# Performance work log

Hardware: AMD Instinct MI355X
Metric: run time of the kernel (lower is better)

The kernel has to match this reference:

```python
import jax, jax.numpy as jnp
import numpy as np

EPS = 1e-5
L = 8      # n_layers
H = 1024   # n_hidden
F_IN = 26  # input features
B = 65536  # batch


def layer_norm(x, gamma, beta):
    m = jnp.mean(x, axis=-1, keepdims=True)
    v = jnp.mean((x - m) ** 2, axis=-1, keepdims=True)
    return (x - m) * jax.lax.rsqrt(v + EPS) * gamma + beta


def setup_inputs() -> dict:
    key = jax.random.key(0)
    ks = jax.random.split(key, 12)
    s_in = 1.0 / np.sqrt(F_IN)
    s_h = 1.0 / np.sqrt(H)
    return {
        "x": jax.random.normal(ks[0], (B, F_IN), jnp.float32),
        "st_gamma": jnp.ones((F_IN,), jnp.float32),
        "st_beta": jnp.zeros((F_IN,), jnp.float32),
        "st_w": jax.random.uniform(ks[1], (H, F_IN), jnp.float32, -s_in, s_in),
        "st_b": jax.random.uniform(ks[2], (H,), jnp.float32, -s_in, s_in),
        "blk_gamma": jnp.ones((L, H), jnp.float32),
        "blk_beta": jnp.zeros((L, H), jnp.float32),
        "blk_w": jax.random.uniform(ks[3], (L, H, H), jnp.float32, -s_h, s_h),
        "blk_b": jax.random.uniform(ks[4], (L, H), jnp.float32, -s_h, s_h),
        "last_gamma": jnp.ones((H,), jnp.float32),
        "last_beta": jnp.zeros((H,), jnp.float32),
        "last_w": jax.random.uniform(ks[5], (1, H), jnp.float32, -s_h, s_h),
        "last_b": jax.random.uniform(ks[6], (1,), jnp.float32, -s_h, s_h),
    }


def reference(x, st_gamma, st_beta, st_w, st_b,
              blk_gamma, blk_beta, blk_w, blk_b,
              last_gamma, last_beta, last_w, last_b):
    # Stem: LN(26) -> Linear(26->H) -> ReLU (dropout = identity in eval)
    h = jax.nn.relu(layer_norm(x, st_gamma, st_beta) @ st_w.T + st_b)

    # n_layers blocks: LN -> Linear(H->H) -> ReLU, scanned over stacked params
    def body(h, params):
        g, b, w, bb = params
        h = jax.nn.relu(layer_norm(h, g, b) @ w.T + bb)
        return h, None

    h, _ = jax.lax.scan(body, h, (blk_gamma, blk_beta, blk_w, blk_b))

    # Head: LN -> Linear(H->1) -> sigmoid
    h = layer_norm(h, last_gamma, last_beta)
    out = jax.nn.sigmoid(h @ last_w.T + last_b)  # [B, 1]
    return out
```

## Files before the change

kernel.cpp:

```cpp
#include <hip/hip_runtime.h>
#include <hip/hip_bf16.h>
#include <stdint.h>


typedef __attribute__((ext_vector_type(8))) _Float16 f16x8;
typedef __attribute__((ext_vector_type(4))) float f32x4;

#define EPSLN 1e-5f
#define HDIM 1024

__device__ __forceinline__ void gload16(const void* g, void* l) {
  __builtin_amdgcn_global_load_lds(
      (const __attribute__((address_space(1))) unsigned int*)g,
      (__attribute__((address_space(3))) unsigned int*)l, 16, 0, 0);
}

__global__ __launch_bounds__(256) void zero_f32(float* __restrict__ p, int n) {
  int i = blockIdx.x * 256 + threadIdx.x;
  if (i < n) p[i] = 0.f;
}

__global__ __launch_bounds__(256) void fold_blk(
    const float* __restrict__ bg, const float* __restrict__ bb,
    const float* __restrict__ bw, const float* __restrict__ bbias,
    float* __restrict__ bfold, float* __restrict__ Sfold) {
  int lo = blockIdx.x;
  int layer = lo >> 10;
  const float* wrow = bw + (size_t)lo * HDIM;
  const float* g = bg + (size_t)layer * HDIM;
  const float* be = bb + (size_t)layer * HDIM;
  int t = threadIdx.x;
  float s = 0.f, acb = 0.f;
  for (int i = t; i < HDIM; i += 256) {
    float wv = wrow[i];
    _Float16 wp = (_Float16)(wv * g[i]);
    s += (float)wp;
    acb += be[i] * wv;
  }
#pragma unroll
  for (int off = 1; off < 64; off <<= 1) { s += __shfl_xor(s, off); acb += __shfl_xor(acb, off); }
  __shared__ float rs[4], rb[4];
  int l = t & 63, w = t >> 6;
  if (l == 0) { rs[w] = s; rb[w] = acb; }
  __syncthreads();
  if (t == 0) {
    Sfold[lo] = rs[0] + rs[1] + rs[2] + rs[3];
    bfold[lo] = bbias[lo] + rb[0] + rb[1] + rb[2] + rb[3];
  }
}

__global__ __launch_bounds__(256) void fold_pack(
    const float* __restrict__ bg, const float* __restrict__ bw,
    _Float16* __restrict__ Wfrag) {
  size_t tid = (size_t)blockIdx.x * 256 + threadIdx.x;
  int lay = (int)(tid >> 17);
  int oct = (int)(tid & 131071);
  int frag = oct >> 6, lane = oct & 63;
  int n16 = frag >> 5, kc = frag & 31;
  int o = n16 * 16 + (lane & 15);
  int ibase = kc * 32 + ((lane >> 4) << 3);
  const float* wrow = bw + ((size_t)lay << 20) + (size_t)o * HDIM + ibase;
  const float* g = bg + (size_t)lay * HDIM + ibase;
  f16x8 v;
#pragma unroll
  for (int j = 0; j < 8; ++j) v[j] = (_Float16)(wrow[j] * g[j]);
  *(f16x8*)(Wfrag + tid * 8) = v;
}

__global__ __launch_bounds__(256) void fold_head(
    const float* __restrict__ lg, const float* __restrict__ lb,
    const float* __restrict__ lw, const float* __restrict__ lbias,
    float* __restrict__ headW, float* __restrict__ headAux) {
  int t = threadIdx.x;
  float s = 0.f, acb = 0.f;
  for (int i = t; i < HDIM; i += 256) {
    float wp = lw[i] * lg[i];
    headW[i] = wp;
    s += wp;
    acb += lb[i] * lw[i];
  }
#pragma unroll
  for (int off = 1; off < 64; off <<= 1) { s += __shfl_xor(s, off); acb += __shfl_xor(acb, off); }
  __shared__ float rs[4], rb[4];
  int l = t & 63, w = t >> 6;
  if (l == 0) { rs[w] = s; rb[w] = acb; }
  __syncthreads();
  if (t == 0) {
    headAux[0] = rs[0] + rs[1] + rs[2] + rs[3];
    headAux[1] = lbias[0] + rb[0] + rb[1] + rb[2] + rb[3];
  }
}

__global__ __launch_bounds__(256) void fold_stem(const float* __restrict__ stw,
                                                 _Float16* __restrict__ Wst) {
  int idx = blockIdx.x * 256 + threadIdx.x;
  int o = idx >> 6, j = idx & 63;
  int i = (((j >> 3) ^ (o & 7)) << 3) + (j & 7);
  Wst[idx] = (i < 26) ? (_Float16)stw[o * 26 + i] : (_Float16)0.f;
}

__global__ __launch_bounds__(256) void stem_gemm(
    const float* __restrict__ x, const float* __restrict__ stg, const float* __restrict__ stb,
    const _Float16* __restrict__ Wst, const float* __restrict__ stbias,
    _Float16* __restrict__ hout, float* __restrict__ stats_out, int rowBase) {
  __shared__ float xin[128 * 26];
  __shared__ _Float16 As[128 * 64];
  __shared__ _Float16 Bs[128 * 64];
  const int t = threadIdx.x;
  const int l = t & 63;
  const int w = t >> 6;
  const int wm = w >> 1, wn = w & 1;
  const int brow = blockIdx.x * 128;
  const int bcol = blockIdx.y * 128;

  const _Float16* gb = Wst + (size_t)(bcol + (t >> 3)) * 64 + (t & 7) * 8;
  char* lB = (char*)Bs + (size_t)w * 1024;
#pragma unroll
  for (int q = 0; q < 4; ++q) gload16(gb + (size_t)q * 32 * 64, lB + q * 4096);

  const float* src = x + ((size_t)rowBase + brow) * 26;
  for (int i = t; i < 128 * 26; i += 256) xin[i] = src[i];
  __syncthreads();

  if (t < 128) {
    float m = 0.f;
#pragma unroll
    for (int i = 0; i < 26; ++i) m += xin[t * 26 + i];
    m *= (1.f / 26.f);
    float v = 0.f;
#pragma unroll
    for (int i = 0; i < 26; ++i) { float d = xin[t * 26 + i] - m; v += d * d; }
    float rstd = rsqrtf(v * (1.f / 26.f) + EPSLN);
    _Float16 tmp[32];
#pragma unroll
    for (int i = 0; i < 26; ++i)
      tmp[i] = (_Float16)((xin[t * 26 + i] - m) * rstd * stg[i] + stb[i]);
#pragma unroll
    for (int i = 26; i < 32; ++i) tmp[i] = (_Float16)0.f;
    char* arow = (char*)As + t * 128;
#pragma unroll
    for (int c = 0; c < 4; ++c) {
      f16x8 vv;
#pragma unroll
      for (int j = 0; j < 8; ++j) vv[j] = tmp[c * 8 + j];
      *(f16x8*)(arow + ((c ^ (t & 7)) << 4)) = vv;
    }
    f16x8 vz = (f16x8)(_Float16)0.f;
#pragma unroll
    for (int c = 4; c < 8; ++c) *(f16x8*)(arow + ((c ^ (t & 7)) << 4)) = vz;
  }
  __syncthreads();

  f32x4 acc[4][4];
#pragma unroll
  for (int i = 0; i < 4; ++i)
#pragma unroll
    for (int j = 0; j < 4; ++j) acc[i][j] = (f32x4){0.f, 0.f, 0.f, 0.f};

#pragma unroll
  for (int ks = 0; ks < 2; ++ks) {
    const int cx = ((ks * 4 + (l >> 4)) ^ (l & 7)) << 4;
    f16x8 af[4], bfr[4];
#pragma unroll
    for (int m = 0; m < 4; ++m)
      af[m] = *(const f16x8*)((const char*)As + (wm * 64 + m * 16 + (l & 15)) * 128 + cx);
#pragma unroll
    for (int n = 0; n < 4; ++n)
      bfr[n] = *(const f16x8*)((const char*)Bs + (wn * 64 + n * 16 + (l & 15)) * 128 + cx);
#pragma unroll
    for (int m = 0; m < 4; ++m)
#pragma unroll
      for (int n = 0; n < 4; ++n)
        acc[m][n] = __builtin_amdgcn_mfma_f32_16x16x32_f16(af[m], bfr[n], acc[m][n], 0, 0, 0);
  }

  __syncthreads();
  float* sred = (float*)xin;
  if (t < 256) sred[t] = 0.f;
  __syncthreads();

  float Bf[4];
#pragma unroll
  for (int n = 0; n < 4; ++n) Bf[n] = stbias[bcol + wn * 64 + n * 16 + (l & 15)];
#pragma unroll
  for (int m = 0; m < 4; ++m) {
#pragma unroll
    for (int rg = 0; rg < 4; ++rg) {
      int rloc = wm * 64 + m * 16 + (l >> 4) * 4 + rg;
      int lrow = brow + rloc;
      float ps = 0.f, psq = 0.f;
#pragma unroll
      for (int n = 0; n < 4; ++n) {
        int col = bcol + wn * 64 + n * 16 + (l & 15);
        float vv = fmaxf(acc[m][n][rg] + Bf[n], 0.f);
        hout[(size_t)lrow * HDIM + col] = (_Float16)vv;
        ps += vv; psq += vv * vv;
      }
#pragma unroll
      for (int off = 1; off < 16; off <<= 1) {
        ps += __shfl_xor(ps, off);
        psq += __shfl_xor(psq, off);
      }
      if ((l & 15) == 0) {
        atomicAdd(&sred[rloc * 2 + 0], ps);
        atomicAdd(&sred[rloc * 2 + 1], psq);
      }
    }
  }
  __syncthreads();
  if (t < 256) atomicAdd(&stats_out[(size_t)(brow + (t >> 1)) * 2 + (t & 1)], sred[t]);
}

__global__ __launch_bounds__(256, 2) void layer_gemm(
    const _Float16* __restrict__ hin, const float* __restrict__ stats_in,
    const _Float16* __restrict__ Wfrag, const float* __restrict__ bfold,
    const float* __restrict__ Sfold, _Float16* __restrict__ hout,
    float* __restrict__ stats_out) {
  __shared__ __align__(128) char smem[2 * 8192];
  const int t = threadIdx.x;
  const int l = t & 63;
  const int w = t >> 6;
  const int wn = w;
  int bid = blockIdx.x;
  {
    int nb = gridDim.x;
    if ((nb & 7) == 0) { int cpx = nb >> 3; bid = (bid & 7) * cpx + (bid >> 3); }
  }
  const int brow = (bid >> 2) * 128;
  const int bcol = (bid & 3) * 256;

  f32x4 acc[8][4];
#pragma unroll
  for (int i = 0; i < 8; ++i)
#pragma unroll
    for (int j = 0; j < 4; ++j) acc[i][j] = (f32x4){0.f, 0.f, 0.f, 0.f};

  const int cswz = (t & 3) ^ ((t >> 3) & 3);
  const _Float16* gA = hin + (size_t)(brow + (t >> 2)) * HDIM + cswz * 8;
  const int dstw = w << 10;

  auto stageA = [&](int kt) {
    char* dA = smem + (kt & 1) * 8192 + dstw;
    const _Float16* sA = gA + kt * 32;
    gload16(sA, dA);
    gload16(sA + (size_t)64 * HDIM, dA + 4096);
  };

  const _Float16* gBf = Wfrag + ((size_t)((bcol >> 4) + wn * 4) * 2048 + l) * 8;

  const int rl = l & 15;
  const int cx = (((l >> 4) ^ ((rl >> 1) & 3)) << 4);
  const int arow0 = rl * 64 + cx;

  f16x8 af[8], bf0[4], bf1[4];

#define LOADB(kt, dst)                                                         \
  do {                                                                         \
    _Pragma("unroll") for (int n = 0; n < 4; ++n)                              \
        dst[n] = *(const f16x8*)(gBf + (size_t)n * 16384 + (kt) * 512);        \
  } while (0)
#define DS_AF(kt)                                                              \
  do {                                                                         \
    const char* bc = smem + ((kt) & 1) * 8192;                                 \
    _Pragma("unroll") for (int m = 0; m < 8; ++m)                              \
        af[m] = *(const f16x8*)(bc + arow0 + m * 1024);                        \
  } while (0)
#define MFMA32(src)                                                            \
  do {                                                                         \
    __builtin_amdgcn_s_setprio(1);                                             \
    _Pragma("unroll") for (int m = 0; m < 8; ++m)                              \
        _Pragma("unroll") for (int n = 0; n < 4; ++n)                          \
            acc[m][n] = __builtin_amdgcn_mfma_f32_16x16x32_f16(af[m], src[n],  \
                                                               acc[m][n], 0, 0, 0); \
    __builtin_amdgcn_s_setprio(0);                                             \
  } while (0)
#define WAIT_PRE(N)                                                            \
  do {                                                                         \
    asm volatile("s_waitcnt vmcnt(" #N ") lgkmcnt(0)" ::: "memory");           \
    __builtin_amdgcn_sched_barrier(0);                                         \
  } while (0)
#define BOUNDARY()                                                             \
  do {                                                                         \
    __builtin_amdgcn_sched_barrier(0);                                         \
    asm volatile("s_waitcnt vmcnt(4)" ::: "memory");                           \
    __builtin_amdgcn_s_barrier();                                              \
    __builtin_amdgcn_sched_barrier(0);                                         \
  } while (0)

  stageA(0);
  LOADB(0, bf0);
  asm volatile("s_waitcnt vmcnt(4)" ::: "memory");
  __builtin_amdgcn_s_barrier();
  __builtin_amdgcn_sched_barrier(0);

#pragma unroll 1
  for (int kt2 = 0; kt2 < 15; ++kt2) {
    const int kt = kt2 * 2;
    stageA(kt + 1);
    LOADB(kt + 1, bf1);
    DS_AF(kt);
    WAIT_PRE(6);
    MFMA32(bf0);
    BOUNDARY();
    stageA(kt + 2);
    LOADB(kt + 2, bf0);
    DS_AF(kt + 1);
    WAIT_PRE(6);
    MFMA32(bf1);
    BOUNDARY();
  }
  stageA(31);
  LOADB(31, bf1);
  DS_AF(30);
  WAIT_PRE(6);
  MFMA32(bf0);
  BOUNDARY();
  DS_AF(31);
  WAIT_PRE(0);
  MFMA32(bf1);
  __syncthreads();

#undef LOADB
#undef DS_AF
#undef MFMA32
#undef WAIT_PRE
#undef BOUNDARY

  float* sred = (float*)smem;
  sred[t] = 0.f;
  __syncthreads();

  float Sf[4], Bf2[4];
#pragma unroll
  for (int n = 0; n < 4; ++n) {
    int col = bcol + wn * 64 + n * 16 + rl;
    Sf[n] = Sfold[col];
    Bf2[n] = bfold[col];
  }
#pragma unroll
  for (int m = 0; m < 8; ++m) {
#pragma unroll
    for (int rg = 0; rg < 4; ++rg) {
      int rloc = m * 16 + (l >> 4) * 4 + rg;
      int grow = brow + rloc;
      float sum = stats_in[(size_t)grow * 2 + 0];
      float sumsq = stats_in[(size_t)grow * 2 + 1];
      float mean = sum * (1.f / 1024.f);
      float rstd = rsqrtf(sumsq * (1.f / 1024.f) - mean * mean + EPSLN);
      float ps = 0.f, psq = 0.f;
#pragma unroll
      for (int n = 0; n < 4; ++n) {
        int col = bcol + wn * 64 + n * 16 + rl;
        float vv = rstd * (acc[m][n][rg] - mean * Sf[n]) + Bf2[n];
        vv = fmaxf(vv, 0.f);
        hout[(size_t)grow * HDIM + col] = (_Float16)vv;
        ps += vv; psq += vv * vv;
      }
#pragma unroll
      for (int off2 = 1; off2 < 16; off2 <<= 1) {
        ps += __shfl_xor(ps, off2);
        psq += __shfl_xor(psq, off2);
      }
      if (rl == 0) {
        atomicAdd(&sred[rloc * 2 + 0], ps);
        atomicAdd(&sred[rloc * 2 + 1], psq);
      }
    }
  }
  __syncthreads();
  atomicAdd(&stats_out[(size_t)(brow + (t >> 1)) * 2 + (t & 1)], sred[t]);
}

__global__ __launch_bounds__(512) void head_kernel(
    const _Float16* __restrict__ h8, const float* __restrict__ stats8,
    const float* __restrict__ headW, const float* __restrict__ headAux,
    float* __restrict__ out, int rowBase) {
  int t = threadIdx.x, l = t & 63, w = t >> 6;
  int lrow = blockIdx.x * 8 + w;
  const f16x8* hp = (const f16x8*)(h8 + (size_t)lrow * HDIM) + l * 2;
  f16x8 v0 = hp[0], v1 = hp[1];
  float acc = 0.f;
#pragma unroll
  for (int j = 0; j < 8; ++j) acc += (float)v0[j] * headW[l * 16 + j];
#pragma unroll
  for (int j = 0; j < 8; ++j) acc += (float)v1[j] * headW[l * 16 + 8 + j];
#pragma unroll
  for (int off = 1; off < 64; off <<= 1) acc += __shfl_xor(acc, off);
  if (l == 0) {
    float sum = stats8[lrow * 2 + 0], sumsq = stats8[lrow * 2 + 1];
    float mean = sum * (1.f / 1024.f);
    float rstd = rsqrtf(sumsq * (1.f / 1024.f) - mean * mean + EPSLN);
    float z = rstd * (acc - mean * headAux[0]) + headAux[1];
    out[rowBase + lrow] = 1.f / (1.f + expf(-z));
  }
}

extern "C" void kernel_launch(void* const* d_in, const int* in_sizes, int n_in,
                              void* d_out, int out_size, void* d_ws, size_t ws_size,
                              hipStream_t stream) {
  const float* x      = (const float*)d_in[0];
  const float* stg    = (const float*)d_in[1];
  const float* stb    = (const float*)d_in[2];
  const float* stw    = (const float*)d_in[3];
  const float* stbias = (const float*)d_in[4];
  const float* bg     = (const float*)d_in[5];
  const float* bb     = (const float*)d_in[6];
  const float* bw     = (const float*)d_in[7];
  const float* bbias  = (const float*)d_in[8];
  const float* lg     = (const float*)d_in[9];
  const float* lb     = (const float*)d_in[10];
  const float* lw     = (const float*)d_in[11];
  const float* lbias  = (const float*)d_in[12];
  float* out = (float*)d_out;
  const int B = 65536;
  const int L = 8;

  char* ws = (char*)d_ws;
  size_t off = 0;
  auto carve = [&](size_t bytes) -> char* {
    char* p = ws + off;
    off = (off + bytes + 255) & ~(size_t)255;
    return p;
  };
  _Float16* Wfrag = (_Float16*)carve((size_t)L * HDIM * HDIM * 2);
  float* bfold   = (float*)carve((size_t)L * HDIM * 4);
  float* Sfold   = (float*)carve((size_t)L * HDIM * 4);
  float* headW   = (float*)carve((size_t)HDIM * 4);
  float* headAux = (float*)carve(256);
  _Float16* Wst  = (_Float16*)carve((size_t)HDIM * 64 * 2);
  size_t fixed = off;

  int R = B;
  while (R > 256) {
    size_t need = fixed + 2 * ((size_t)R * HDIM * 2 + 256) + ((size_t)9 * R * 2 * 4 + 256);
    if (need <= ws_size) break;
    R >>= 1;
  }
  _Float16* hA = (_Float16*)carve((size_t)R * HDIM * 2);
  _Float16* hB = (_Float16*)carve((size_t)R * HDIM * 2);
  float* stats = (float*)carve((size_t)9 * R * 2 * 4);

  fold_blk<<<L * HDIM, 256, 0, stream>>>(bg, bb, bw, bbias, bfold, Sfold);
  fold_pack<<<(L * 131072) / 256, 256, 0, stream>>>(bg, bw, Wfrag);
  fold_head<<<1, 256, 0, stream>>>(lg, lb, lw, lbias, headW, headAux);
  fold_stem<<<HDIM * 64 / 256, 256, 0, stream>>>(stw, Wst);

  const int nstats = 9 * R * 2;
  for (int c = 0; c < B / R; ++c) {
    int rowBase = c * R;
    zero_f32<<<(nstats + 255) / 256, 256, 0, stream>>>(stats, nstats);
    {
      dim3 grid(R / 128, 8);
      stem_gemm<<<grid, 256, 0, stream>>>(x, stg, stb, Wst, stbias, hA, stats, rowBase);
    }
    _Float16* cur = hA;
    _Float16* nxt = hB;
    for (int lyr = 0; lyr < L; ++lyr) {
      int nb = (R / 128) * 4;
      layer_gemm<<<nb, 256, 0, stream>>>(
          cur, stats + (size_t)lyr * R * 2, Wfrag + (size_t)lyr * HDIM * HDIM,
          bfold + lyr * HDIM, Sfold + lyr * HDIM, nxt, stats + (size_t)(lyr + 1) * R * 2);
      _Float16* tmp = cur; cur = nxt; nxt = tmp;
    }
    head_kernel<<<R / 8, 512, 0, stream>>>(cur, stats + (size_t)8 * R * 2, headW, headAux, out, rowBase);
  }
}
```

Baseline: 1.410 ms.

## Shrink layer GEMM tile to 128x128 with 2x2 warps and higher occupancy

Each layer_gemm block now computes a 128x128 output tile instead of 128x256, with four warps arranged 2x2 so each warp holds 64x64 accumulators instead of 128x64. The launch bound goes from 2 to 4 blocks per SIMD and the grid doubles. The double-buffered B-register pipeline is replaced by a single-buffer loop that issues B loads in the same iteration they are consumed. The aim is to rely on higher occupancy to hide latency while cutting register pressure. The cost is less data reuse per warp, more A/B traffic, and global-load latency that is no longer software-prefetched.

```diff
diff --git a/kernel.cpp b/kernel.cpp
--- a/kernel.cpp
+++ b/kernel.cpp
@@ -211,7 +211,7 @@
   if (t < 256) atomicAdd(&stats_out[(size_t)(brow + (t >> 1)) * 2 + (t & 1)], sred[t]);
 }
 
-__global__ __launch_bounds__(256, 2) void layer_gemm(
+__global__ __launch_bounds__(256, 4) void layer_gemm(
     const _Float16* __restrict__ hin, const float* __restrict__ stats_in,
     const _Float16* __restrict__ Wfrag, const float* __restrict__ bfold,
     const float* __restrict__ Sfold, _Float16* __restrict__ hout,
@@ -220,18 +220,18 @@
   const int t = threadIdx.x;
   const int l = t & 63;
   const int w = t >> 6;
-  const int wn = w;
+  const int wm = w >> 1, wn = w & 1;
   int bid = blockIdx.x;
   {
     int nb = gridDim.x;
     if ((nb & 7) == 0) { int cpx = nb >> 3; bid = (bid & 7) * cpx + (bid >> 3); }
   }
-  const int brow = (bid >> 2) * 128;
-  const int bcol = (bid & 3) * 256;
-
-  f32x4 acc[8][4];
-#pragma unroll
-  for (int i = 0; i < 8; ++i)
+  const int brow = (bid >> 3) * 128;
+  const int bcol = (bid & 7) * 128;
+
+  f32x4 acc[4][4];
+#pragma unroll
+  for (int i = 0; i < 4; ++i)
 #pragma unroll
     for (int j = 0; j < 4; ++j) acc[i][j] = (f32x4){0.f, 0.f, 0.f, 0.f};
 
@@ -250,81 +250,59 @@
 
   const int rl = l & 15;
   const int cx = (((l >> 4) ^ ((rl >> 1) & 3)) << 4);
-  const int arow0 = rl * 64 + cx;
-
-  f16x8 af[8], bf0[4], bf1[4];
-
-#define LOADB(kt, dst)                                                         \
+  const int arow0 = wm * 4096 + rl * 64 + cx;
+
+  f16x8 af[4], bf[4];
+
+#define LOADB(kt)                                                              \
   do {                                                                         \
     _Pragma("unroll") for (int n = 0; n < 4; ++n)                              \
-        dst[n] = *(const f16x8*)(gBf + (size_t)n * 16384 + (kt) * 512);        \
+        bf[n] = *(const f16x8*)(gBf + (size_t)n * 16384 + (kt) * 512);         \
   } while (0)
 #define DS_AF(kt)                                                              \
   do {                                                                         \
     const char* bc = smem + ((kt) & 1) * 8192;                                 \
-    _Pragma("unroll") for (int m = 0; m < 8; ++m)                              \
+    _Pragma("unroll") for (int m = 0; m < 4; ++m)                              \
         af[m] = *(const f16x8*)(bc + arow0 + m * 1024);                        \
   } while (0)
-#define MFMA32(src)                                                            \
+#define MFMA16()                                                               \
   do {                                                                         \
     __builtin_amdgcn_s_setprio(1);                                             \
-    _Pragma("unroll") for (int m = 0; m < 8; ++m)                              \
+    _Pragma("unroll") for (int m = 0; m < 4; ++m)                              \
         _Pragma("unroll") for (int n = 0; n < 4; ++n)                          \
-            acc[m][n] = __builtin_amdgcn_mfma_f32_16x16x32_f16(af[m], src[n],  \
+            acc[m][n] = __builtin_amdgcn_mfma_f32_16x16x32_f16(af[m], bf[n],   \
                                                                acc[m][n], 0, 0, 0); \
     __builtin_amdgcn_s_setprio(0);                                             \
   } while (0)
-#define WAIT_PRE(N)                                                            \
-  do {                                                                         \
-    asm volatile("s_waitcnt vmcnt(" #N ") lgkmcnt(0)" ::: "memory");           \
-    __builtin_amdgcn_sched_barrier(0);                                         \
-  } while (0)
-#define BOUNDARY()                                                             \
-  do {                                                                         \
-    __builtin_amdgcn_sched_barrier(0);                                         \
-    asm volatile("s_waitcnt vmcnt(4)" ::: "memory");                           \
-    __builtin_amdgcn_s_barrier();                                              \
-    __builtin_amdgcn_sched_barrier(0);                                         \
-  } while (0)
 
   stageA(0);
-  LOADB(0, bf0);
-  asm volatile("s_waitcnt vmcnt(4)" ::: "memory");
+  asm volatile("s_waitcnt vmcnt(0)" ::: "memory");
   __builtin_amdgcn_s_barrier();
   __builtin_amdgcn_sched_barrier(0);
 
 #pragma unroll 1
-  for (int kt2 = 0; kt2 < 15; ++kt2) {
-    const int kt = kt2 * 2;
+  for (int kt = 0; kt < 31; ++kt) {
+    LOADB(kt);
     stageA(kt + 1);
-    LOADB(kt + 1, bf1);
     DS_AF(kt);
-    WAIT_PRE(6);
-    MFMA32(bf0);
-    BOUNDARY();
-    stageA(kt + 2);
-    LOADB(kt + 2, bf0);
-    DS_AF(kt + 1);
-    WAIT_PRE(6);
-    MFMA32(bf1);
-    BOUNDARY();
-  }
-  stageA(31);
-  LOADB(31, bf1);
-  DS_AF(30);
-  WAIT_PRE(6);
-  MFMA32(bf0);
-  BOUNDARY();
+    asm volatile("s_waitcnt vmcnt(2) lgkmcnt(0)" ::: "memory");
+    __builtin_amdgcn_sched_barrier(0);
+    MFMA16();
+    __builtin_amdgcn_sched_barrier(0);
+    asm volatile("s_waitcnt vmcnt(0)" ::: "memory");
+    __builtin_amdgcn_s_barrier();
+    __builtin_amdgcn_sched_barrier(0);
+  }
+  LOADB(31);
   DS_AF(31);
-  WAIT_PRE(0);
-  MFMA32(bf1);
+  asm volatile("s_waitcnt vmcnt(0) lgkmcnt(0)" ::: "memory");
+  __builtin_amdgcn_sched_barrier(0);
+  MFMA16();
   __syncthreads();
 
 #undef LOADB
 #undef DS_AF
-#undef MFMA32
-#undef WAIT_PRE
-#undef BOUNDARY
+#undef MFMA16
 
   float* sred = (float*)smem;
   sred[t] = 0.f;
@@ -338,10 +316,10 @@
     Bf2[n] = bfold[col];
   }
 #pragma unroll
-  for (int m = 0; m < 8; ++m) {
+  for (int m = 0; m < 4; ++m) {
 #pragma unroll
     for (int rg = 0; rg < 4; ++rg) {
-      int rloc = m * 16 + (l >> 4) * 4 + rg;
+      int rloc = wm * 64 + m * 16 + (l >> 4) * 4 + rg;
       int grow = brow + rloc;
       float sum = stats_in[(size_t)grow * 2 + 0];
       float sumsq = stats_in[(size_t)grow * 2 + 1];
@@ -456,7 +434,7 @@
     _Float16* cur = hA;
     _Float16* nxt = hB;
     for (int lyr = 0; lyr < L; ++lyr) {
-      int nb = (R / 128) * 4;
+      int nb = (R / 128) * 8;
       layer_gemm<<<nb, 256, 0, stream>>>(
           cur, stats + (size_t)lyr * R * 2, Wfrag + (size_t)lyr * HDIM * HDIM,
           bfold + lyr * HDIM, Sfold + lyr * HDIM, nxt, stats + (size_t)(lyr + 1) * R * 2);
```

New measurement: 1.469 ms. 1.04x slower.
